# Optimization experiments

Measured on AMD Instinct MI355X. Metric: run time of the kernel, lower is better.

Reference implementation:

```python
import jax, jax.numpy as jnp
import numpy as np

IN_F = 4096
OUT_F = 11008
GROUP = 128
NGROUPS = IN_F // GROUP
MAX_INT = 15  # 2**4 - 1


def setup_inputs() -> dict:
    key = jax.random.key(0)
    k1, k2, k3, k4, k5 = jax.random.split(key, 5)
    x = jax.random.normal(k1, (4, 2048, IN_F), dtype=jnp.float32)
    qweight = jax.random.randint(k2, (OUT_F, IN_F), 0, MAX_INT + 1, dtype=jnp.int32)
    scales = jax.random.uniform(k3, (OUT_F, NGROUPS), dtype=jnp.float32) * 0.01 + 1e-4
    zeros = jax.random.uniform(k4, (OUT_F, NGROUPS), dtype=jnp.float32) * MAX_INT
    b = jax.random.normal(k5, (OUT_F,), dtype=jnp.float32)
    return {"x": x, "qweight": qweight, "scales": scales, "zeros": zeros, "b": b}


def reference(x, qweight, scales, zeros, b):
    # Group-wise dequantization: W[o, i] = (q[o, i] - zeros[o, g(i)]) * scales[o, g(i)]
    s_rep = jnp.repeat(scales, GROUP, axis=1)  # [OUT_F, IN_F]
    z_rep = jnp.repeat(zeros, GROUP, axis=1)   # [OUT_F, IN_F]
    w_fp = (qweight.astype(x.dtype) - z_rep.astype(x.dtype)) * s_rep.astype(x.dtype)
    # F.linear: x @ W.T + b
    out = jnp.einsum('bsi,oi->bso', x, w_fp) + b.astype(x.dtype)
    return out
```

## Files before the change

kernel.cpp:

```cpp
#include <hip/hip_runtime.h>
#include <hip/hip_bf16.h>


#define K_DIM 4096
#define N_DIM 11008
#define M_DIM 8192
#define NGRP 32

typedef __bf16 bf16x8 __attribute__((ext_vector_type(8)));
typedef float f32x4 __attribute__((ext_vector_type(4)));
typedef unsigned short u16x8 __attribute__((ext_vector_type(8)));

__device__ __forceinline__ unsigned short f2bf(float f) {
  unsigned u = __builtin_bit_cast(unsigned, f);
  return (unsigned short)((u + 0x7FFFu + ((u >> 16) & 1u)) >> 16);
}

__device__ __forceinline__ void gload_lds16(const void* g, void* l) {
  __builtin_amdgcn_global_load_lds(
      (const __attribute__((address_space(1))) unsigned int*)(unsigned long long)g,
      (__attribute__((address_space(3))) unsigned int*)(unsigned int)(unsigned long long)l,
      16, 0, 0);
}

__global__ __launch_bounds__(256) void cvt_x_kernel(const float4* __restrict__ x4,
                                                    u16x8* __restrict__ xb) {
  int i = blockIdx.x * 256 + threadIdx.x;
  float4 a = x4[2 * i], b = x4[2 * i + 1];
  u16x8 r;
  r[0] = f2bf(a.x); r[1] = f2bf(a.y); r[2] = f2bf(a.z); r[3] = f2bf(a.w);
  r[4] = f2bf(b.x); r[5] = f2bf(b.y); r[6] = f2bf(b.z); r[7] = f2bf(b.w);
  xb[i] = r;
}

__global__ __launch_bounds__(256) void dequant_kernel(const int4* __restrict__ q4,
                                                      const float* __restrict__ scales,
                                                      const float* __restrict__ zeros,
                                                      u16x8* __restrict__ wb) {
  int t = blockIdx.x * 256 + threadIdx.x;
  int o = t >> 9;
  int j8 = t & 511;
  int g = j8 >> 4;
  float s = scales[o * NGRP + g];
  float z = zeros[o * NGRP + g];
  float nzs = -z * s;
  int4 qa = q4[2 * t], qb = q4[2 * t + 1];
  u16x8 r;
  r[0] = f2bf(fmaf((float)qa.x, s, nzs));
  r[1] = f2bf(fmaf((float)qa.y, s, nzs));
  r[2] = f2bf(fmaf((float)qa.z, s, nzs));
  r[3] = f2bf(fmaf((float)qa.w, s, nzs));
  r[4] = f2bf(fmaf((float)qb.x, s, nzs));
  r[5] = f2bf(fmaf((float)qb.y, s, nzs));
  r[6] = f2bf(fmaf((float)qb.z, s, nzs));
  r[7] = f2bf(fmaf((float)qb.w, s, nzs));
  wb[t] = r;
}

#define BAR() __builtin_amdgcn_s_barrier()
#define SCHED0() __builtin_amdgcn_sched_barrier(0)

__global__ __launch_bounds__(512, 2) void gemm_kernel(const unsigned short* __restrict__ A,
                                                      const unsigned short* __restrict__ B,
                                                      const float* __restrict__ bias,
                                                      float* __restrict__ C) {
  extern __shared__ unsigned short smem[];
  unsigned short* sAb = smem;
  unsigned short* sBb = smem + 32768;

  const int bid = blockIdx.x;
  const int swz = (bid & 7) * 172 + (bid >> 3);
  const int tm = swz / 43, tn = swz % 43;

  const int tid = threadIdx.x;
  const int w = tid >> 6, l = tid & 63;
  const int wr = w >> 2, wc = w & 3;

  const int dsto = w * 512 + l * 8;
  const int gs = (l & 7) ^ (l >> 3);
  const unsigned short* gA = A + (size_t)(tm * 256 + (tid >> 3)) * K_DIM + gs * 8;
  const unsigned short* gB = B + (size_t)(tn * 256 + (tid >> 3)) * K_DIM + gs * 8;

#define STG_A(tt, h, dst)                                                       \
  do {                                                                          \
    const unsigned short* _s = gA + (size_t)(h) * 128 * K_DIM + (tt) * 64;      \
    gload_lds16(_s, (dst) + dsto);                                              \
    gload_lds16(_s + 64 * K_DIM, (dst) + 4096 + dsto);                          \
  } while (0)
#define STG_B(tt, h, dst)                                                       \
  do {                                                                          \
    const unsigned short* _s = gB + (size_t)(h) * 128 * K_DIM + (tt) * 64;      \
    gload_lds16(_s, (dst) + dsto);                                              \
    gload_lds16(_s + 64 * K_DIM, (dst) + 4096 + dsto);                          \
  } while (0)

  const int fr = l & 15, sb = l >> 4, x7 = l & 7;
  const int abase = (wr * 64 + fr) * 64;
  const int bbase = (wc * 32 + fr) * 64;
  const int k0 = (sb ^ x7) * 8;
  const int k1 = ((sb + 4) ^ x7) * 8;

  bf16x8 av[4][2], bva[2][2], bvb[2][2];
  f32x4 acc[8][4] = {};

#define READ_A(half)                                                     \
  {                                                                      \
    _Pragma("unroll") for (int m = 0; m < 4; ++m) {                      \
      av[m][0] = *(const bf16x8*)((half) + abase + m * 1024 + k0);       \
      av[m][1] = *(const bf16x8*)((half) + abase + m * 1024 + k1);       \
    }                                                                    \
  }
#define READ_B(half, arr)                                                \
  {                                                                      \
    _Pragma("unroll") for (int n = 0; n < 2; ++n) {                      \
      arr[n][0] = *(const bf16x8*)((half) + bbase + n * 1024 + k0);      \
      arr[n][1] = *(const bf16x8*)((half) + bbase + n * 1024 + k1);      \
    }                                                                    \
  }
#define MFMA_Q(mh, nh, arr)                                                        \
  {                                                                                \
    __builtin_amdgcn_s_setprio(1);                                                 \
    _Pragma("unroll") for (int kk = 0; kk < 2; ++kk)                               \
    _Pragma("unroll") for (int m = 0; m < 4; ++m)                                  \
    _Pragma("unroll") for (int nn = 0; nn < 2; ++nn)                               \
      acc[(mh)*4 + m][(nh)*2 + nn] = __builtin_amdgcn_mfma_f32_16x16x32_bf16(      \
          av[m][kk], arr[nn][kk], acc[(mh)*4 + m][(nh)*2 + nn], 0, 0, 0);          \
    __builtin_amdgcn_s_setprio(0);                                                 \
  }

  STG_A(0, 0, sAb);
  STG_A(0, 1, sAb + 8192);
  STG_B(0, 0, sBb);
  STG_B(0, 1, sBb + 8192);
  STG_A(1, 0, sAb + 16384);
  STG_B(1, 1, sBb + 16384 + 8192);
  asm volatile("s_waitcnt vmcnt(4)" ::: "memory");
  BAR();
  SCHED0();

  for (int tt = 0; tt < 32; ++tt) {
    READ_A(sAb);
    READ_B(sBb, bva);
    READ_B(sBb + 8192, bvb);
    STG_A(2 * tt + 1, 1, sAb + 16384 + 8192);
    STG_B(2 * tt + 1, 0, sBb + 16384);
    SCHED0();
    BAR();
    SCHED0();
    MFMA_Q(0, 0, bva);
    MFMA_Q(0, 1, bvb);
    READ_A(sAb + 8192);
    if (tt < 31) {
      STG_A(2 * tt + 2, 0, sAb);
      STG_B(2 * tt + 2, 1, sBb + 8192);
    }
    if (tt < 31) {
      asm volatile("s_waitcnt vmcnt(4)" ::: "memory");
    } else {
      asm volatile("s_waitcnt vmcnt(0)" ::: "memory");
    }
    SCHED0();
    BAR();
    SCHED0();
    MFMA_Q(1, 1, bvb);
    MFMA_Q(1, 0, bva);

    READ_A(sAb + 16384);
    READ_B(sBb + 16384, bva);
    READ_B(sBb + 16384 + 8192, bvb);
    if (tt < 31) {
      STG_A(2 * tt + 2, 1, sAb + 8192);
      STG_B(2 * tt + 2, 0, sBb);
    }
    SCHED0();
    BAR();
    SCHED0();
    MFMA_Q(0, 0, bva);
    MFMA_Q(0, 1, bvb);
    READ_A(sAb + 16384 + 8192);
    if (tt < 31) {
      STG_A(2 * tt + 3, 0, sAb + 16384);
      STG_B(2 * tt + 3, 1, sBb + 16384 + 8192);
    }
    if (tt < 31) {
      asm volatile("s_waitcnt vmcnt(4)" ::: "memory");
      SCHED0();
      BAR();
      SCHED0();
    }
    MFMA_Q(1, 1, bvb);
    MFMA_Q(1, 0, bva);
  }

  const int r0 = tm * 256 + wr * 64 + sb * 4;
  const int c0 = tn * 256 + wc * 32 + fr;
#pragma unroll
  for (int n = 0; n < 4; ++n) {
    const int col = c0 + (n >> 1) * 128 + (n & 1) * 16;
    const float bv = bias[col];
#pragma unroll
    for (int mi = 0; mi < 8; ++mi) {
      const int row = r0 + (mi >> 2) * 128 + (mi & 3) * 16;
#pragma unroll
      for (int jj = 0; jj < 4; ++jj)
        C[(size_t)(row + jj) * N_DIM + col] = acc[mi][n][jj] + bv;
    }
  }
}

extern "C" void kernel_launch(void* const* d_in, const int* in_sizes, int n_in,
                              void* d_out, int out_size, void* d_ws, size_t ws_size,
                              hipStream_t stream) {
  const float* x = (const float*)d_in[0];
  const int* qw = (const int*)d_in[1];
  const float* sc = (const float*)d_in[2];
  const float* zr = (const float*)d_in[3];
  const float* bs = (const float*)d_in[4];
  float* out = (float*)d_out;

  const size_t xb_bytes = (size_t)M_DIM * K_DIM * 2;
  const size_t wb_bytes = (size_t)N_DIM * K_DIM * 2;
  if (ws_size < xb_bytes + wb_bytes) return;

  unsigned short* xb = (unsigned short*)d_ws;
  unsigned short* wb = (unsigned short*)((char*)d_ws + xb_bytes);

  (void)hipFuncSetAttribute((const void*)gemm_kernel,
                            hipFuncAttributeMaxDynamicSharedMemorySize, 131072);

  cvt_x_kernel<<<(M_DIM * K_DIM / 8) / 256, 256, 0, stream>>>((const float4*)x, (u16x8*)xb);
  dequant_kernel<<<(N_DIM * K_DIM / 8) / 256, 256, 0, stream>>>((const int4*)qw, sc, zr,
                                                                (u16x8*)wb);
  gemm_kernel<<<(M_DIM / 256) * (N_DIM / 256), 512, 131072, stream>>>(xb, wb, bs, out);
}
```

Before: 710.3 us.

## Split-K the tail wave of GEMM tiles with atomic accumulation

The GEMM grid has 1376 tiles. The first 1280 are computed normally, and the remaining 96 tail tiles are each split into two K-halves run by separate blocks (192 blocks). Each half atomically adds into a pre-zeroed output with half the bias, and a new kernel zeroes those tail tiles beforehand. The intent is to balance the last wave across the GPU's CUs instead of leaving most idle. The cost is an extra zeroing kernel launch, atomic global adds on the tail, and float summation order that varies between runs.

```diff
diff --git a/kernel.cpp b/kernel.cpp
--- a/kernel.cpp
+++ b/kernel.cpp
@@ -57,6 +57,17 @@
   wb[t] = r;
 }
 
+__global__ __launch_bounds__(256) void ztail_kernel(float* __restrict__ C) {
+  int i = blockIdx.x * 256 + threadIdx.x;
+  int r = i >> 16;
+  int w = i & 65535;
+  int tile = 1280 + r;
+  int swz = (tile & 7) * 172 + (tile >> 3);
+  int tm = swz / 43, tn = swz % 43;
+  int row = w >> 8, col = w & 255;
+  C[(size_t)(tm * 256 + row) * N_DIM + (tn * 256 + col)] = 0.f;
+}
+
 #define BAR() __builtin_amdgcn_s_barrier()
 #define SCHED0() __builtin_amdgcn_sched_barrier(0)
 
@@ -68,8 +79,20 @@
   unsigned short* sAb = smem;
   unsigned short* sBb = smem + 32768;
 
-  const int bid = blockIdx.x;
-  const int swz = (bid & 7) * 172 + (bid >> 3);
+  const int j = blockIdx.x;
+  int tileIdx, k0i, nhalf;
+  bool isFull;
+  if (j < 1280) {
+    tileIdx = j; k0i = 0; nhalf = 32; isFull = true;
+  } else {
+    int r = j - 1280;
+    tileIdx = 1280 + (r % 96);
+    k0i = (r / 96) * 32;
+    nhalf = 16; isFull = false;
+  }
+  const int lim = nhalf - 1;
+
+  const int swz = (tileIdx & 7) * 172 + (tileIdx >> 3);
   const int tm = swz / 43, tn = swz % 43;
 
   const int tid = threadIdx.x;
@@ -128,33 +151,35 @@
     __builtin_amdgcn_s_setprio(0);                                                 \
   }
 
-  STG_A(0, 0, sAb);
-  STG_A(0, 1, sAb + 8192);
-  STG_B(0, 0, sBb);
-  STG_B(0, 1, sBb + 8192);
-  STG_A(1, 0, sAb + 16384);
-  STG_B(1, 1, sBb + 16384 + 8192);
+  STG_A(k0i, 0, sAb);
+  STG_A(k0i, 1, sAb + 8192);
+  STG_B(k0i, 0, sBb);
+  STG_B(k0i, 1, sBb + 8192);
+  STG_A(k0i + 1, 0, sAb + 16384);
+  STG_B(k0i + 1, 1, sBb + 16384 + 8192);
   asm volatile("s_waitcnt vmcnt(4)" ::: "memory");
   BAR();
   SCHED0();
 
-  for (int tt = 0; tt < 32; ++tt) {
+  for (int tt = 0; tt < nhalf; ++tt) {
+    const int te = k0i + 2 * tt;
+
     READ_A(sAb);
     READ_B(sBb, bva);
     READ_B(sBb + 8192, bvb);
-    STG_A(2 * tt + 1, 1, sAb + 16384 + 8192);
-    STG_B(2 * tt + 1, 0, sBb + 16384);
+    STG_A(te + 1, 1, sAb + 16384 + 8192);
+    STG_B(te + 1, 0, sBb + 16384);
     SCHED0();
     BAR();
     SCHED0();
     MFMA_Q(0, 0, bva);
     MFMA_Q(0, 1, bvb);
     READ_A(sAb + 8192);
-    if (tt < 31) {
-      STG_A(2 * tt + 2, 0, sAb);
-      STG_B(2 * tt + 2, 1, sBb + 8192);
-    }
-    if (tt < 31) {
+    if (tt < lim) {
+      STG_A(te + 2, 0, sAb);
+      STG_B(te + 2, 1, sBb + 8192);
+    }
+    if (tt < lim) {
       asm volatile("s_waitcnt vmcnt(4)" ::: "memory");
     } else {
       asm volatile("s_waitcnt vmcnt(0)" ::: "memory");
@@ -168,9 +193,9 @@
     READ_A(sAb + 16384);
     READ_B(sBb + 16384, bva);
     READ_B(sBb + 16384 + 8192, bvb);
-    if (tt < 31) {
-      STG_A(2 * tt + 2, 1, sAb + 8192);
-      STG_B(2 * tt + 2, 0, sBb);
+    if (tt < lim) {
+      STG_A(te + 2, 1, sAb + 8192);
+      STG_B(te + 2, 0, sBb);
     }
     SCHED0();
     BAR();
@@ -178,11 +203,11 @@
     MFMA_Q(0, 0, bva);
     MFMA_Q(0, 1, bvb);
     READ_A(sAb + 16384 + 8192);
-    if (tt < 31) {
-      STG_A(2 * tt + 3, 0, sAb + 16384);
-      STG_B(2 * tt + 3, 1, sBb + 16384 + 8192);
-    }
-    if (tt < 31) {
+    if (tt < lim) {
+      STG_A(te + 3, 0, sAb + 16384);
+      STG_B(te + 3, 1, sBb + 16384 + 8192);
+    }
+    if (tt < lim) {
       asm volatile("s_waitcnt vmcnt(4)" ::: "memory");
       SCHED0();
       BAR();
@@ -194,16 +219,23 @@
 
   const int r0 = tm * 256 + wr * 64 + sb * 4;
   const int c0 = tn * 256 + wc * 32 + fr;
+  const float bsc = isFull ? 1.0f : 0.5f;
 #pragma unroll
   for (int n = 0; n < 4; ++n) {
     const int col = c0 + (n >> 1) * 128 + (n & 1) * 16;
-    const float bv = bias[col];
+    const float bv = bias[col] * bsc;
 #pragma unroll
     for (int mi = 0; mi < 8; ++mi) {
       const int row = r0 + (mi >> 2) * 128 + (mi & 3) * 16;
-#pragma unroll
-      for (int jj = 0; jj < 4; ++jj)
-        C[(size_t)(row + jj) * N_DIM + col] = acc[mi][n][jj] + bv;
+      if (isFull) {
+#pragma unroll
+        for (int jj = 0; jj < 4; ++jj)
+          C[(size_t)(row + jj) * N_DIM + col] = acc[mi][n][jj] + bv;
+      } else {
+#pragma unroll
+        for (int jj = 0; jj < 4; ++jj)
+          atomicAdd(&C[(size_t)(row + jj) * N_DIM + col], acc[mi][n][jj] + bv);
+      }
     }
   }
 }
@@ -231,5 +263,6 @@
   cvt_x_kernel<<<(M_DIM * K_DIM / 8) / 256, 256, 0, stream>>>((const float4*)x, (u16x8*)xb);
   dequant_kernel<<<(N_DIM * K_DIM / 8) / 256, 256, 0, stream>>>((const int4*)qw, sc, zr,
                                                                 (u16x8*)wb);
-  gemm_kernel<<<(M_DIM / 256) * (N_DIM / 256), 512, 131072, stream>>>(xb, wb, bs, out);
-}
+  ztail_kernel<<<(96 * 65536) / 256, 256, 0, stream>>>(out);
+  gemm_kernel<<<1280 + 192, 512, 131072, stream>>>(xb, wb, bs, out);
+}
```

Result: slower. 737.7 us (+3.9%).

## Switch GEMM to 32x32x16 MFMA and fuse prep kernels into one launch

Applied to the files above, without the earlier changes.

The GEMM inner loop now uses 32x32x16 bf16 MFMA instructions with larger register fragments in place of 16x16x32. This reduces LDS fragment reads per MFMA and changes the accumulator layout, and the output epilogue is remapped to match. The x conversion and weight dequantization kernels are merged into a single launch that branches on block index, saving one launch. Register pressure from the 16-wide accumulators may affect occupancy.

```diff
diff --git a/kernel.cpp b/kernel.cpp
--- a/kernel.cpp
+++ b/kernel.cpp
@@ -8,7 +8,7 @@
 #define NGRP 32
 
 typedef __bf16 bf16x8 __attribute__((ext_vector_type(8)));
-typedef float f32x4 __attribute__((ext_vector_type(4)));
+typedef float f32x16 __attribute__((ext_vector_type(16)));
 typedef unsigned short u16x8 __attribute__((ext_vector_type(8)));
 
 __device__ __forceinline__ unsigned short f2bf(float f) {
@@ -23,38 +23,40 @@
       16, 0, 0);
 }
 
-__global__ __launch_bounds__(256) void cvt_x_kernel(const float4* __restrict__ x4,
-                                                    u16x8* __restrict__ xb) {
-  int i = blockIdx.x * 256 + threadIdx.x;
-  float4 a = x4[2 * i], b = x4[2 * i + 1];
-  u16x8 r;
-  r[0] = f2bf(a.x); r[1] = f2bf(a.y); r[2] = f2bf(a.z); r[3] = f2bf(a.w);
-  r[4] = f2bf(b.x); r[5] = f2bf(b.y); r[6] = f2bf(b.z); r[7] = f2bf(b.w);
-  xb[i] = r;
-}
-
-__global__ __launch_bounds__(256) void dequant_kernel(const int4* __restrict__ q4,
-                                                      const float* __restrict__ scales,
-                                                      const float* __restrict__ zeros,
-                                                      u16x8* __restrict__ wb) {
-  int t = blockIdx.x * 256 + threadIdx.x;
-  int o = t >> 9;
-  int j8 = t & 511;
-  int g = j8 >> 4;
-  float s = scales[o * NGRP + g];
-  float z = zeros[o * NGRP + g];
-  float nzs = -z * s;
-  int4 qa = q4[2 * t], qb = q4[2 * t + 1];
-  u16x8 r;
-  r[0] = f2bf(fmaf((float)qa.x, s, nzs));
-  r[1] = f2bf(fmaf((float)qa.y, s, nzs));
-  r[2] = f2bf(fmaf((float)qa.z, s, nzs));
-  r[3] = f2bf(fmaf((float)qa.w, s, nzs));
-  r[4] = f2bf(fmaf((float)qb.x, s, nzs));
-  r[5] = f2bf(fmaf((float)qb.y, s, nzs));
-  r[6] = f2bf(fmaf((float)qb.z, s, nzs));
-  r[7] = f2bf(fmaf((float)qb.w, s, nzs));
-  wb[t] = r;
+__global__ __launch_bounds__(256) void prep_kernel(const float4* __restrict__ x4,
+                                                   const int4* __restrict__ q4,
+                                                   const float* __restrict__ scales,
+                                                   const float* __restrict__ zeros,
+                                                   u16x8* __restrict__ xb,
+                                                   u16x8* __restrict__ wb) {
+  const int bid = blockIdx.x;
+  if (bid < 16384) {
+    int i = bid * 256 + threadIdx.x;
+    float4 a = x4[2 * i], b = x4[2 * i + 1];
+    u16x8 r;
+    r[0] = f2bf(a.x); r[1] = f2bf(a.y); r[2] = f2bf(a.z); r[3] = f2bf(a.w);
+    r[4] = f2bf(b.x); r[5] = f2bf(b.y); r[6] = f2bf(b.z); r[7] = f2bf(b.w);
+    xb[i] = r;
+  } else {
+    int t = (bid - 16384) * 256 + threadIdx.x;
+    int o = t >> 9;
+    int j8 = t & 511;
+    int g = j8 >> 4;
+    float s = scales[o * NGRP + g];
+    float z = zeros[o * NGRP + g];
+    float nzs = -z * s;
+    int4 qa = q4[2 * t], qb = q4[2 * t + 1];
+    u16x8 r;
+    r[0] = f2bf(fmaf((float)qa.x, s, nzs));
+    r[1] = f2bf(fmaf((float)qa.y, s, nzs));
+    r[2] = f2bf(fmaf((float)qa.z, s, nzs));
+    r[3] = f2bf(fmaf((float)qa.w, s, nzs));
+    r[4] = f2bf(fmaf((float)qb.x, s, nzs));
+    r[5] = f2bf(fmaf((float)qb.y, s, nzs));
+    r[6] = f2bf(fmaf((float)qb.z, s, nzs));
+    r[7] = f2bf(fmaf((float)qb.w, s, nzs));
+    wb[t] = r;
+  }
 }
 
 #define BAR() __builtin_amdgcn_s_barrier()
@@ -94,38 +96,41 @@
     gload_lds16(_s + 64 * K_DIM, (dst) + 4096 + dsto);                          \
   } while (0)
 
-  const int fr = l & 15, sb = l >> 4, x7 = l & 7;
-  const int abase = (wr * 64 + fr) * 64;
-  const int bbase = (wc * 32 + fr) * 64;
-  const int k0 = (sb ^ x7) * 8;
-  const int k1 = ((sb + 4) ^ x7) * 8;
-
-  bf16x8 av[4][2], bva[2][2], bvb[2][2];
-  f32x4 acc[8][4] = {};
-
-#define READ_A(half)                                                     \
-  {                                                                      \
-    _Pragma("unroll") for (int m = 0; m < 4; ++m) {                      \
-      av[m][0] = *(const bf16x8*)((half) + abase + m * 1024 + k0);       \
-      av[m][1] = *(const bf16x8*)((half) + abase + m * 1024 + k1);       \
-    }                                                                    \
-  }
-#define READ_B(half, arr)                                                \
-  {                                                                      \
-    _Pragma("unroll") for (int n = 0; n < 2; ++n) {                      \
-      arr[n][0] = *(const bf16x8*)((half) + bbase + n * 1024 + k0);      \
-      arr[n][1] = *(const bf16x8*)((half) + bbase + n * 1024 + k1);      \
-    }                                                                    \
-  }
-#define MFMA_Q(mh, nh, arr)                                                        \
-  {                                                                                \
-    __builtin_amdgcn_s_setprio(1);                                                 \
-    _Pragma("unroll") for (int kk = 0; kk < 2; ++kk)                               \
-    _Pragma("unroll") for (int m = 0; m < 4; ++m)                                  \
-    _Pragma("unroll") for (int nn = 0; nn < 2; ++nn)                               \
-      acc[(mh)*4 + m][(nh)*2 + nn] = __builtin_amdgcn_mfma_f32_16x16x32_bf16(      \
-          av[m][kk], arr[nn][kk], acc[(mh)*4 + m][(nh)*2 + nn], 0, 0, 0);          \
-    __builtin_amdgcn_s_setprio(0);                                                 \
+  const int l31 = l & 31, lk = l >> 5, x7 = l & 7;
+  const int sl0 = (0 + lk) ^ x7;
+  const int sl1 = (2 + lk) ^ x7;
+  const int sl2 = (4 + lk) ^ x7;
+  const int sl3 = (6 + lk) ^ x7;
+  const int abase = (wr * 64 + l31) * 64;
+  const int bbase = (wc * 32 + l31) * 64;
+
+  bf16x8 avv[2][4], bv0[4], bv1[4];
+  f32x16 acc[4][2] = {};
+
+#define READ_A(half)                                                       \
+  {                                                                        \
+    _Pragma("unroll") for (int mf = 0; mf < 2; ++mf) {                     \
+      avv[mf][0] = *(const bf16x8*)((half) + abase + mf * 2048 + sl0 * 8); \
+      avv[mf][1] = *(const bf16x8*)((half) + abase + mf * 2048 + sl1 * 8); \
+      avv[mf][2] = *(const bf16x8*)((half) + abase + mf * 2048 + sl2 * 8); \
+      avv[mf][3] = *(const bf16x8*)((half) + abase + mf * 2048 + sl3 * 8); \
+    }                                                                      \
+  }
+#define READ_B(half, arr)                                                  \
+  {                                                                        \
+    arr[0] = *(const bf16x8*)((half) + bbase + sl0 * 8);                   \
+    arr[1] = *(const bf16x8*)((half) + bbase + sl1 * 8);                   \
+    arr[2] = *(const bf16x8*)((half) + bbase + sl2 * 8);                   \
+    arr[3] = *(const bf16x8*)((half) + bbase + sl3 * 8);                   \
+  }
+#define MFMA_Q(ha, hb, barr)                                                        \
+  {                                                                                 \
+    __builtin_amdgcn_s_setprio(1);                                                  \
+    _Pragma("unroll") for (int ks = 0; ks < 4; ++ks)                                \
+    _Pragma("unroll") for (int mf = 0; mf < 2; ++mf)                                \
+      acc[(ha)*2 + mf][hb] = __builtin_amdgcn_mfma_f32_32x32x16_bf16(               \
+          avv[mf][ks], barr[ks], acc[(ha)*2 + mf][hb], 0, 0, 0);                    \
+    __builtin_amdgcn_s_setprio(0);                                                  \
   }
 
   STG_A(0, 0, sAb);
@@ -140,15 +145,15 @@
 
   for (int tt = 0; tt < 32; ++tt) {
     READ_A(sAb);
-    READ_B(sBb, bva);
-    READ_B(sBb + 8192, bvb);
+    READ_B(sBb, bv0);
+    READ_B(sBb + 8192, bv1);
     STG_A(2 * tt + 1, 1, sAb + 16384 + 8192);
     STG_B(2 * tt + 1, 0, sBb + 16384);
     SCHED0();
     BAR();
     SCHED0();
-    MFMA_Q(0, 0, bva);
-    MFMA_Q(0, 1, bvb);
+    MFMA_Q(0, 0, bv0);
+    MFMA_Q(0, 1, bv1);
     READ_A(sAb + 8192);
     if (tt < 31) {
       STG_A(2 * tt + 2, 0, sAb);
@@ -162,12 +167,12 @@
     SCHED0();
     BAR();
     SCHED0();
-    MFMA_Q(1, 1, bvb);
-    MFMA_Q(1, 0, bva);
+    MFMA_Q(1, 1, bv1);
+    MFMA_Q(1, 0, bv0);
 
     READ_A(sAb + 16384);
-    READ_B(sBb + 16384, bva);
-    READ_B(sBb + 16384 + 8192, bvb);
+    READ_B(sBb + 16384, bv0);
+    READ_B(sBb + 16384 + 8192, bv1);
     if (tt < 31) {
       STG_A(2 * tt + 2, 1, sAb + 8192);
       STG_B(2 * tt + 2, 0, sBb);
@@ -175,8 +180,8 @@
     SCHED0();
     BAR();
     SCHED0();
-    MFMA_Q(0, 0, bva);
-    MFMA_Q(0, 1, bvb);
+    MFMA_Q(0, 0, bv0);
+    MFMA_Q(0, 1, bv1);
     READ_A(sAb + 16384 + 8192);
     if (tt < 31) {
       STG_A(2 * tt + 3, 0, sAb + 16384);
@@ -188,22 +193,24 @@
       BAR();
       SCHED0();
     }
-    MFMA_Q(1, 1, bvb);
-    MFMA_Q(1, 0, bva);
-  }
-
-  const int r0 = tm * 256 + wr * 64 + sb * 4;
-  const int c0 = tn * 256 + wc * 32 + fr;
+    MFMA_Q(1, 1, bv1);
+    MFMA_Q(1, 0, bv0);
+  }
+
+  const int r0 = tm * 256 + wr * 64 + 4 * lk;
+  const int c0 = tn * 256 + wc * 32 + l31;
 #pragma unroll
-  for (int n = 0; n < 4; ++n) {
-    const int col = c0 + (n >> 1) * 128 + (n & 1) * 16;
-    const float bv = bias[col];
+  for (int hb = 0; hb < 2; ++hb) {
+    const int col = c0 + hb * 128;
+    const float bvl = bias[col];
 #pragma unroll
-    for (int mi = 0; mi < 8; ++mi) {
-      const int row = r0 + (mi >> 2) * 128 + (mi & 3) * 16;
+    for (int mi = 0; mi < 4; ++mi) {
+      const int rowb = r0 + (mi >> 1) * 128 + (mi & 1) * 32;
 #pragma unroll
-      for (int jj = 0; jj < 4; ++jj)
-        C[(size_t)(row + jj) * N_DIM + col] = acc[mi][n][jj] + bv;
+      for (int reg = 0; reg < 16; ++reg) {
+        const int row = rowb + (reg & 3) + 8 * (reg >> 2);
+        C[(size_t)row * N_DIM + col] = acc[mi][hb][reg] + bvl;
+      }
     }
   }
 }
@@ -228,8 +235,7 @@
   (void)hipFuncSetAttribute((const void*)gemm_kernel,
                             hipFuncAttributeMaxDynamicSharedMemorySize, 131072);
 
-  cvt_x_kernel<<<(M_DIM * K_DIM / 8) / 256, 256, 0, stream>>>((const float4*)x, (u16x8*)xb);
-  dequant_kernel<<<(N_DIM * K_DIM / 8) / 256, 256, 0, stream>>>((const int4*)qw, sc, zr,
-                                                                (u16x8*)wb);
+  prep_kernel<<<16384 + 22016, 256, 0, stream>>>((const float4*)x, (const int4*)qw, sc, zr,
+                                                 (u16x8*)xb, (u16x8*)wb);
   gemm_kernel<<<(M_DIM / 256) * (N_DIM / 256), 512, 131072, stream>>>(xb, wb, bs, out);
 }
```

Result: slower. 769.5 us (+8.3%).

## Split tail GEMM tiles into half-N blocks and merge prep kernels

Applied to the files above, without the earlier changes.

Merges the x conversion and weight dequantization into one launch, removing a kernel boundary. The GEMM now runs the first 1280 tiles as full 256x256 blocks and splits the remaining 96 tiles into two blocks, each computing one 128-column half, so the final wave spreads over more CUs. The split blocks still load the full B tile and all of A, which adds redundant memory traffic and divergent control flow inside the main loop.

```diff
diff --git a/kernel.cpp b/kernel.cpp
--- a/kernel.cpp
+++ b/kernel.cpp
@@ -23,38 +23,40 @@
       16, 0, 0);
 }
 
-__global__ __launch_bounds__(256) void cvt_x_kernel(const float4* __restrict__ x4,
-                                                    u16x8* __restrict__ xb) {
-  int i = blockIdx.x * 256 + threadIdx.x;
-  float4 a = x4[2 * i], b = x4[2 * i + 1];
-  u16x8 r;
-  r[0] = f2bf(a.x); r[1] = f2bf(a.y); r[2] = f2bf(a.z); r[3] = f2bf(a.w);
-  r[4] = f2bf(b.x); r[5] = f2bf(b.y); r[6] = f2bf(b.z); r[7] = f2bf(b.w);
-  xb[i] = r;
-}
-
-__global__ __launch_bounds__(256) void dequant_kernel(const int4* __restrict__ q4,
-                                                      const float* __restrict__ scales,
-                                                      const float* __restrict__ zeros,
-                                                      u16x8* __restrict__ wb) {
-  int t = blockIdx.x * 256 + threadIdx.x;
-  int o = t >> 9;
-  int j8 = t & 511;
-  int g = j8 >> 4;
-  float s = scales[o * NGRP + g];
-  float z = zeros[o * NGRP + g];
-  float nzs = -z * s;
-  int4 qa = q4[2 * t], qb = q4[2 * t + 1];
-  u16x8 r;
-  r[0] = f2bf(fmaf((float)qa.x, s, nzs));
-  r[1] = f2bf(fmaf((float)qa.y, s, nzs));
-  r[2] = f2bf(fmaf((float)qa.z, s, nzs));
-  r[3] = f2bf(fmaf((float)qa.w, s, nzs));
-  r[4] = f2bf(fmaf((float)qb.x, s, nzs));
-  r[5] = f2bf(fmaf((float)qb.y, s, nzs));
-  r[6] = f2bf(fmaf((float)qb.z, s, nzs));
-  r[7] = f2bf(fmaf((float)qb.w, s, nzs));
-  wb[t] = r;
+__global__ __launch_bounds__(256) void prep_kernel(const float4* __restrict__ x4,
+                                                   const int4* __restrict__ q4,
+                                                   const float* __restrict__ scales,
+                                                   const float* __restrict__ zeros,
+                                                   u16x8* __restrict__ xb,
+                                                   u16x8* __restrict__ wb) {
+  const int bid = blockIdx.x;
+  if (bid < 16384) {
+    int i = bid * 256 + threadIdx.x;
+    float4 a = x4[2 * i], b = x4[2 * i + 1];
+    u16x8 r;
+    r[0] = f2bf(a.x); r[1] = f2bf(a.y); r[2] = f2bf(a.z); r[3] = f2bf(a.w);
+    r[4] = f2bf(b.x); r[5] = f2bf(b.y); r[6] = f2bf(b.z); r[7] = f2bf(b.w);
+    xb[i] = r;
+  } else {
+    int t = (bid - 16384) * 256 + threadIdx.x;
+    int o = t >> 9;
+    int j8 = t & 511;
+    int g = j8 >> 4;
+    float s = scales[o * NGRP + g];
+    float z = zeros[o * NGRP + g];
+    float nzs = -z * s;
+    int4 qa = q4[2 * t], qb = q4[2 * t + 1];
+    u16x8 r;
+    r[0] = f2bf(fmaf((float)qa.x, s, nzs));
+    r[1] = f2bf(fmaf((float)qa.y, s, nzs));
+    r[2] = f2bf(fmaf((float)qa.z, s, nzs));
+    r[3] = f2bf(fmaf((float)qa.w, s, nzs));
+    r[4] = f2bf(fmaf((float)qb.x, s, nzs));
+    r[5] = f2bf(fmaf((float)qb.y, s, nzs));
+    r[6] = f2bf(fmaf((float)qb.z, s, nzs));
+    r[7] = f2bf(fmaf((float)qb.w, s, nzs));
+    wb[t] = r;
+  }
 }
 
 #define BAR() __builtin_amdgcn_s_barrier()
@@ -68,8 +70,19 @@
   unsigned short* sAb = smem;
   unsigned short* sBb = smem + 32768;
 
-  const int bid = blockIdx.x;
-  const int swz = (bid & 7) * 172 + (bid >> 3);
+  const int j = blockIdx.x;
+  int tileIdx, nh;
+  bool isFull;
+  if (j < 1280) {
+    tileIdx = j; nh = 0; isFull = true;
+  } else {
+    int r = j - 1280;
+    tileIdx = 1280 + (r % 96);
+    nh = r / 96;
+    isFull = false;
+  }
+
+  const int swz = (tileIdx & 7) * 172 + (tileIdx >> 3);
   const int tm = swz / 43, tn = swz % 43;
 
   const int tid = threadIdx.x;
@@ -117,16 +130,19 @@
       arr[n][1] = *(const bf16x8*)((half) + bbase + n * 1024 + k1);      \
     }                                                                    \
   }
-#define MFMA_Q(mh, nh, arr)                                                        \
+#define MFMA_Q(mh, nhq, arr)                                                       \
   {                                                                                \
     __builtin_amdgcn_s_setprio(1);                                                 \
     _Pragma("unroll") for (int kk = 0; kk < 2; ++kk)                               \
     _Pragma("unroll") for (int m = 0; m < 4; ++m)                                  \
     _Pragma("unroll") for (int nn = 0; nn < 2; ++nn)                               \
-      acc[(mh)*4 + m][(nh)*2 + nn] = __builtin_amdgcn_mfma_f32_16x16x32_bf16(      \
-          av[m][kk], arr[nn][kk], acc[(mh)*4 + m][(nh)*2 + nn], 0, 0, 0);          \
+      acc[(mh)*4 + m][(nhq)*2 + nn] = __builtin_amdgcn_mfma_f32_16x16x32_bf16(     \
+          av[m][kk], arr[nn][kk], acc[(mh)*4 + m][(nhq)*2 + nn], 0, 0, 0);         \
     __builtin_amdgcn_s_setprio(0);                                                 \
   }
+
+  const bool doB0 = isFull || (nh == 0);
+  const bool doB1 = isFull || (nh == 1);
 
   STG_A(0, 0, sAb);
   STG_A(0, 1, sAb + 8192);
@@ -140,15 +156,15 @@
 
   for (int tt = 0; tt < 32; ++tt) {
     READ_A(sAb);
-    READ_B(sBb, bva);
-    READ_B(sBb + 8192, bvb);
+    if (doB0) READ_B(sBb, bva);
+    if (doB1) READ_B(sBb + 8192, bvb);
     STG_A(2 * tt + 1, 1, sAb + 16384 + 8192);
     STG_B(2 * tt + 1, 0, sBb + 16384);
     SCHED0();
     BAR();
     SCHED0();
-    MFMA_Q(0, 0, bva);
-    MFMA_Q(0, 1, bvb);
+    if (doB0) MFMA_Q(0, 0, bva);
+    if (doB1) MFMA_Q(0, 1, bvb);
     READ_A(sAb + 8192);
     if (tt < 31) {
       STG_A(2 * tt + 2, 0, sAb);
@@ -162,12 +178,12 @@
     SCHED0();
     BAR();
     SCHED0();
-    MFMA_Q(1, 1, bvb);
-    MFMA_Q(1, 0, bva);
+    if (doB1) MFMA_Q(1, 1, bvb);
+    if (doB0) MFMA_Q(1, 0, bva);
 
     READ_A(sAb + 16384);
-    READ_B(sBb + 16384, bva);
-    READ_B(sBb + 16384 + 8192, bvb);
+    if (doB0) READ_B(sBb + 16384, bva);
+    if (doB1) READ_B(sBb + 16384 + 8192, bvb);
     if (tt < 31) {
       STG_A(2 * tt + 2, 1, sAb + 8192);
       STG_B(2 * tt + 2, 0, sBb);
@@ -175,8 +191,8 @@
     SCHED0();
     BAR();
     SCHED0();
-    MFMA_Q(0, 0, bva);
-    MFMA_Q(0, 1, bvb);
+    if (doB0) MFMA_Q(0, 0, bva);
+    if (doB1) MFMA_Q(0, 1, bvb);
     READ_A(sAb + 16384 + 8192);
     if (tt < 31) {
       STG_A(2 * tt + 3, 0, sAb + 16384);
@@ -188,14 +204,15 @@
       BAR();
       SCHED0();
     }
-    MFMA_Q(1, 1, bvb);
-    MFMA_Q(1, 0, bva);
+    if (doB1) MFMA_Q(1, 1, bvb);
+    if (doB0) MFMA_Q(1, 0, bva);
   }
 
   const int r0 = tm * 256 + wr * 64 + sb * 4;
   const int c0 = tn * 256 + wc * 32 + fr;
 #pragma unroll
   for (int n = 0; n < 4; ++n) {
+    if (!isFull && (n >> 1) != nh) continue;
     const int col = c0 + (n >> 1) * 128 + (n & 1) * 16;
     const float bv = bias[col];
 #pragma unroll
@@ -228,8 +245,7 @@
   (void)hipFuncSetAttribute((const void*)gemm_kernel,
                             hipFuncAttributeMaxDynamicSharedMemorySize, 131072);
 
-  cvt_x_kernel<<<(M_DIM * K_DIM / 8) / 256, 256, 0, stream>>>((const float4*)x, (u16x8*)xb);
-  dequant_kernel<<<(N_DIM * K_DIM / 8) / 256, 256, 0, stream>>>((const int4*)qw, sc, zr,
-                                                                (u16x8*)wb);
-  gemm_kernel<<<(M_DIM / 256) * (N_DIM / 256), 512, 131072, stream>>>(xb, wb, bs, out);
-}
+  prep_kernel<<<16384 + 22016, 256, 0, stream>>>((const float4*)x, (const int4*)qw, sc, zr,
+                                                 (u16x8*)xb, (u16x8*)wb);
+  gemm_kernel<<<1280 + 192, 512, 131072, stream>>>(xb, wb, bs, out);
+}
```

Result: no change. 716.4 us (+0.9%).
